# Optimization experiments

Measured on AMD Instinct MI355X. Metric: run time of the kernel, lower is better.

## Reference

```python
import jax, jax.numpy as jnp
import numpy as np

N_S, N_D, E, L = 10000, 2000, 100000, 50000
H = 8            # attention heads
H1, H2, H3 = 128, 128, 64
D_S, D_D = 128, 64
NEG_SLOPE = 0.2  # GATv2 leaky_relu slope


def setup_inputs() -> dict:
    key = jax.random.key(0)
    ks = iter(jax.random.split(key, 48))
    def nrm(shape, fan_in):
        return (jax.random.normal(next(ks), shape) / np.sqrt(fan_in)).astype(jnp.float32)
    inp = {}
    inp["x_snorna"] = jax.random.normal(next(ks), (N_S, D_S), dtype=jnp.float32)
    inp["x_disease"] = jax.random.normal(next(ks), (N_D, D_D), dtype=jnp.float32)
    inp["edge_src"] = jax.random.randint(next(ks), (E,), 0, N_S, dtype=jnp.int32)
    inp["edge_dst"] = jax.random.randint(next(ks), (E,), 0, N_D, dtype=jnp.int32)
    inp["edge_label_src"] = jax.random.randint(next(ks), (L,), 0, N_S, dtype=jnp.int32)
    inp["edge_label_dst"] = jax.random.randint(next(ks), (L,), 0, N_D, dtype=jnp.int32)
    # layer 1: GraphConv per relation (lin_rel has bias, lin_root no bias)
    inp["W1_rel_sd"] = nrm((D_S, H1), D_S); inp["b1_sd"] = jnp.zeros((H1,), jnp.float32)
    inp["W1_root_sd"] = nrm((D_D, H1), D_D)
    inp["W1_rel_ds"] = nrm((D_D, H1), D_D); inp["b1_ds"] = jnp.zeros((H1,), jnp.float32)
    inp["W1_root_ds"] = nrm((D_S, H1), D_S)
    # layer 2: GATv2Conv per relation (lin_l/lin_r with bias, att, final bias)
    for rel in ("sd", "ds"):
        inp[f"Wl2_{rel}"] = nrm((H1, H * H2), H1); inp[f"bl2_{rel}"] = jnp.zeros((H * H2,), jnp.float32)
        inp[f"Wr2_{rel}"] = nrm((H1, H * H2), H1); inp[f"br2_{rel}"] = jnp.zeros((H * H2,), jnp.float32)
        inp[f"att2_{rel}"] = nrm((H, H2), H2)
        inp[f"bias2_{rel}"] = jnp.zeros((H2,), jnp.float32)
    # layer 3: GraphConv per relation
    inp["W3_rel_sd"] = nrm((H2, H3), H2); inp["b3_sd"] = jnp.zeros((H3,), jnp.float32)
    inp["W3_root_sd"] = nrm((H2, H3), H2)
    inp["W3_rel_ds"] = nrm((H2, H3), H2); inp["b3_ds"] = jnp.zeros((H3,), jnp.float32)
    inp["W3_root_ds"] = nrm((H2, H3), H2)
    return inp


def graph_conv(x_src, x_dst, es, ed, W_rel, b_rel, W_root, n_dst):
    # PyG GraphConv: lin_rel(sum-aggregated neighbor feats) + lin_root(x_dst)
    agg = jax.ops.segment_sum(x_src[es], ed, num_segments=n_dst)
    return agg @ W_rel + b_rel + x_dst @ W_root


def gatv2(x_src, x_dst, es, ed, Wl, bl, Wr, br, att, bias, n_dst):
    # PyG GATv2Conv, bipartite, add_self_loops=False, concat=False (mean over heads)
    xl = (x_src @ Wl + bl).reshape(x_src.shape[0], H, -1)  # [Ns,H,C]
    xr = (x_dst @ Wr + br).reshape(x_dst.shape[0], H, -1)  # [Nd,H,C]
    xj = xl[es]                                            # [E,H,C] source msgs
    e = jax.nn.leaky_relu(xj + xr[ed], NEG_SLOPE)          # [E,H,C]
    score = jnp.einsum('ehc,hc->eh', e, att)               # [E,H]
    m = jax.ops.segment_max(score, ed, num_segments=n_dst)
    a = jnp.exp(score - m[ed])
    denom = jax.ops.segment_sum(a, ed, num_segments=n_dst)
    alpha = a / denom[ed]                                  # softmax over in-edges of dst
    out = jax.ops.segment_sum(alpha[:, :, None] * xj, ed, num_segments=n_dst)
    return out.mean(axis=1) + bias                         # concat=False -> head mean


def reference(x_snorna, x_disease, edge_src, edge_dst, edge_label_src, edge_label_dst,
              W1_rel_sd, b1_sd, W1_root_sd, W1_rel_ds, b1_ds, W1_root_ds,
              Wl2_sd, bl2_sd, Wr2_sd, br2_sd, att2_sd, bias2_sd,
              Wl2_ds, bl2_ds, Wr2_ds, br2_ds, att2_ds, bias2_ds,
              W3_rel_sd, b3_sd, W3_root_sd, W3_rel_ds, b3_ds, W3_root_ds):
    # HeteroConv layer 1 (GraphConv both directions); each type has one incoming relation
    xd = graph_conv(x_snorna, x_disease, edge_src, edge_dst, W1_rel_sd, b1_sd, W1_root_sd, N_D)
    xs = graph_conv(x_disease, x_snorna, edge_dst, edge_src, W1_rel_ds, b1_ds, W1_root_ds, N_S)
    xs, xd = jax.nn.relu(xs), jax.nn.relu(xd)  # dropout = identity (eval mode)
    # HeteroConv layer 2 (GATv2Conv both directions)
    xd2 = gatv2(xs, xd, edge_src, edge_dst, Wl2_sd, bl2_sd, Wr2_sd, br2_sd, att2_sd, bias2_sd, N_D)
    xs2 = gatv2(xd, xs, edge_dst, edge_src, Wl2_ds, bl2_ds, Wr2_ds, br2_ds, att2_ds, bias2_ds, N_S)
    xs2, xd2 = jax.nn.relu(xs2), jax.nn.relu(xd2)
    # HeteroConv layer 3 (GraphConv, no activation)
    xd3 = graph_conv(xs2, xd2, edge_src, edge_dst, W3_rel_sd, b3_sd, W3_root_sd, N_D)
    xs3 = graph_conv(xd2, xs2, edge_dst, edge_src, W3_rel_ds, b3_ds, W3_root_ds, N_S)
    # Classifier: per-pair dot product
    return (xs3[edge_label_src] * xd3[edge_label_dst]).sum(axis=-1)
```

## Files before the change

### kernel.cpp

```cpp
#include <hip/hip_runtime.h>
#include <math.h>

#define NEG 0.2f
static const int N_S = 10000, N_D = 2000, E_N = 100000, L_N = 50000;

using short8 = __attribute__((ext_vector_type(8))) short;
using f32x4  = __attribute__((ext_vector_type(4))) float;
typedef _Float16 h2 __attribute__((ext_vector_type(2)));

union U8h { uint4 u[2]; h2 h[8]; unsigned w[8]; };

__device__ inline unsigned short f2bf(float f) {
  unsigned u = __float_as_uint(f);
  u += 0x7fff + ((u >> 16) & 1);
  return (unsigned short)(u >> 16);
}
__device__ inline float bf2f(unsigned short u) {
  return __uint_as_float((unsigned)u << 16);
}
__device__ inline unsigned short f2h(float f) {
  _Float16 h = (_Float16)f;
  unsigned short r;
  __builtin_memcpy(&r, &h, 2);
  return r;
}

struct PkD { const float* W; unsigned short* P; int K, M; };
struct Pk12 { PkD d[12]; };
struct PrepArgs {
  const int *es, *ed;
  int *deg_s, *deg_d;
  const float *xs, *xd;
  unsigned short *xsb, *xdb;
  const float *att_sd, *att_ds;
  unsigned short *att16;
};
__global__ void k_prep(PrepArgs a, Pk12 g) {
  int bid = blockIdx.x, t = threadIdx.x;
  if (bid < 391) {
    int e = bid * 256 + t;
    if (e < E_N) {
      atomicAdd(&a.deg_d[a.ed[e]], 1);
      atomicAdd(&a.deg_s[a.es[e]], 1);
    }
  } else if (bid < 391 + 1375) {
    int i = (bid - 391) * 256 + t;
    const int ns4 = N_S * 32;
    if (i < ns4) {
      float4 v = ((const float4*)a.xs)[i];
      ushort4 o = {f2bf(v.x), f2bf(v.y), f2bf(v.z), f2bf(v.w)};
      ((ushort4*)a.xsb)[i] = o;
    } else {
      int j = i - ns4;
      float4 v = ((const float4*)a.xd)[j];
      ushort4 o = {f2bf(v.x), f2bf(v.y), f2bf(v.z), f2bf(v.w)};
      ((ushort4*)a.xdb)[j] = o;
    }
  } else if (bid < 391 + 1375 + 768) {
    int sub = bid - 391 - 1375;
    PkD d = g.d[sub >> 6];
    int total = d.K * d.M, mt = d.M >> 4;
    for (int tid = (sub & 63) * 256 + t; tid < total; tid += 64 * 256) {
      int r = tid & 7, l = (tid >> 3) & 63, rest = tid >> 9;
      int ct = rest % mt, kt = rest / mt;
      d.P[tid] = f2bf(d.W[(kt * 32 + (l >> 4) * 8 + r) * d.M + ct * 16 + (l & 15)]);
    }
  } else {
    int i = (bid - 391 - 1375 - 768) * 256 + t;
    float v = (i < 1024) ? a.att_sd[i] : a.att_ds[i - 1024];
    a.att16[i] = f2h(v);
  }
}

__global__ __launch_bounds__(1024) void k_scan2(int* c0, int* r0, int n0,
                                                int* c1, int* r1, int n1) {
  int* cur = blockIdx.x ? c1 : c0;
  int* rp  = blockIdx.x ? r1 : r0;
  int N    = blockIdx.x ? n1 : n0;
  __shared__ int wsum[16];
  __shared__ int carry;
  if (threadIdx.x == 0) carry = 0;
  __syncthreads();
  int lane = threadIdx.x & 63, wid = threadIdx.x >> 6;
  for (int base = 0; base < N; base += 1024) {
    int i = base + threadIdx.x;
    int v = (i < N) ? cur[i] : 0;
    int x = v;
    #pragma unroll
    for (int dd = 1; dd < 64; dd <<= 1) {
      int t = __shfl_up(x, dd);
      if (lane >= dd) x += t;
    }
    if (lane == 63) wsum[wid] = x;
    __syncthreads();
    int woff = 0;
    for (int ww = 0; ww < wid; ++ww) woff += wsum[ww];
    int excl = carry + woff + x - v;
    if (i < N) { rp[i] = excl; cur[i] = excl; }
    __syncthreads();
    if (threadIdx.x == 0) {
      int t = 0;
      #pragma unroll
      for (int ww = 0; ww < 16; ++ww) t += wsum[ww];
      if (base + 1024 >= N) rp[N] = carry + t;
      carry += t;
    }
    __syncthreads();
  }
}

__global__ void k_scat2(const int* __restrict__ es, const int* __restrict__ ed,
                        int* __restrict__ cur_d, int* __restrict__ cur_s,
                        int* __restrict__ csrc_d, int* __restrict__ csrc_s, int E) {
  int e = blockIdx.x * 256 + threadIdx.x;
  if (e >= E) return;
  int s = es[e], d = ed[e];
  csrc_d[atomicAdd(&cur_d[d], 1)] = s;
  csrc_s[atomicAdd(&cur_s[s], 1)] = d;
}

__device__ __forceinline__ void gath128(const unsigned short* __restrict__ x,
                                        const int* __restrict__ rp, const int* __restrict__ cs,
                                        unsigned short* __restrict__ out,
                                        int n, int half, int cl) {
  int b = rp[n], e = rp[n + 1];
  float a0 = 0.f, a1 = 0.f, a2 = 0.f, a3 = 0.f;
  int i = b + half;
  for (; i + 2 < e; i += 4) {
    uint2 v0 = *(const uint2*)(x + (long long)cs[i] * 128 + cl * 4);
    uint2 v1 = *(const uint2*)(x + (long long)cs[i + 2] * 128 + cl * 4);
    a0 += bf2f((unsigned short)(v0.x & 0xffff)) + bf2f((unsigned short)(v1.x & 0xffff));
    a1 += bf2f((unsigned short)(v0.x >> 16))    + bf2f((unsigned short)(v1.x >> 16));
    a2 += bf2f((unsigned short)(v0.y & 0xffff)) + bf2f((unsigned short)(v1.y & 0xffff));
    a3 += bf2f((unsigned short)(v0.y >> 16))    + bf2f((unsigned short)(v1.y >> 16));
  }
  for (; i < e; i += 2) {
    uint2 v0 = *(const uint2*)(x + (long long)cs[i] * 128 + cl * 4);
    a0 += bf2f((unsigned short)(v0.x & 0xffff));
    a1 += bf2f((unsigned short)(v0.x >> 16));
    a2 += bf2f((unsigned short)(v0.y & 0xffff));
    a3 += bf2f((unsigned short)(v0.y >> 16));
  }
  a0 += __shfl_xor(a0, 32); a1 += __shfl_xor(a1, 32);
  a2 += __shfl_xor(a2, 32); a3 += __shfl_xor(a3, 32);
  if (!half) {
    ushort4 o = {f2bf(a0), f2bf(a1), f2bf(a2), f2bf(a3)};
    *(ushort4*)&out[(long long)n * 128 + cl * 4] = o;
  }
}

__global__ __launch_bounds__(256) void k_gather1(
    const unsigned short* __restrict__ xsb, const unsigned short* __restrict__ xdb,
    const int* __restrict__ rpd, const int* __restrict__ csd,
    const int* __restrict__ rps, const int* __restrict__ css,
    unsigned short* __restrict__ aggd, unsigned short* __restrict__ aggs) {
  int wv = threadIdx.x >> 6, l = threadIdx.x & 63, half = l >> 5, cl = l & 31;
  int bid = blockIdx.x;
  if (bid < 500) {
    gath128(xsb, rpd, csd, aggd, bid * 4 + wv, half, cl);
  } else {
    int n = (bid - 500) * 4 + wv;
    if (n >= N_S) return;
    int b = rps[n], e = rps[n + 1];
    float a0 = 0.f, a1 = 0.f;
    int i = b + half;
    for (; i + 2 < e; i += 4) {
      unsigned v0 = *(const unsigned*)(xdb + (long long)css[i] * 64 + cl * 2);
      unsigned v1 = *(const unsigned*)(xdb + (long long)css[i + 2] * 64 + cl * 2);
      a0 += bf2f((unsigned short)(v0 & 0xffff)) + bf2f((unsigned short)(v1 & 0xffff));
      a1 += bf2f((unsigned short)(v0 >> 16))    + bf2f((unsigned short)(v1 >> 16));
    }
    for (; i < e; i += 2) {
      unsigned v0 = *(const unsigned*)(xdb + (long long)css[i] * 64 + cl * 2);
      a0 += bf2f((unsigned short)(v0 & 0xffff));
      a1 += bf2f((unsigned short)(v0 >> 16));
    }
    a0 += __shfl_xor(a0, 32); a1 += __shfl_xor(a1, 32);
    if (!half) {
      ushort2 o = {f2bf(a0), f2bf(a1)};
      *(ushort2*)&aggs[(long long)n * 64 + cl * 2] = o;
    }
  }
}

__global__ __launch_bounds__(256) void k_gather3(
    const unsigned short* __restrict__ xs2b, const unsigned short* __restrict__ xd2b,
    const int* __restrict__ rpd, const int* __restrict__ csd,
    const int* __restrict__ rps, const int* __restrict__ css,
    unsigned short* __restrict__ aggd, unsigned short* __restrict__ aggs) {
  int wv = threadIdx.x >> 6, l = threadIdx.x & 63, half = l >> 5, cl = l & 31;
  int bid = blockIdx.x;
  if (bid < 500) {
    gath128(xs2b, rpd, csd, aggd, bid * 4 + wv, half, cl);
  } else {
    int n = (bid - 500) * 4 + wv;
    if (n >= N_S) return;
    gath128(xd2b, rps, css, aggs, n, half, cl);
  }
}

struct GD {
  const unsigned short *A0, *P0, *A1, *P1;
  const float* bias;
  void* out;
  int K0, K1, N, M, relu, outmode, y0;
};
template<int ND> struct GDs { GD d[ND]; };

template<int ND>
__global__ __launch_bounds__(256) void k_mfma(GDs<ND> g) {
  int by = blockIdx.y;
  int di = 0;
  #pragma unroll
  for (int i = 1; i < ND; ++i) if (by >= g.d[i].y0) di = i;
  GD d = g.d[di];
  int ytile = by - d.y0;
  int c0 = blockIdx.x * 64;
  if (c0 >= d.M) return;
  int w = threadIdx.x >> 6, l = threadIdx.x & 63;
  int r0 = ytile * 64 + w * 16;
  if (r0 >= d.N) return;
  int lg = l >> 4, lo = l & 15;
  f32x4 acc[4] = {};
  int arow = r0 + lo; arow = (arow < d.N) ? arow : (d.N - 1);
  int mt = d.M >> 4;
  int ct0 = c0 >> 4;
  const unsigned short* a0 = d.A0 + (long long)arow * d.K0 + lg * 8;
  for (int kt = 0; kt < (d.K0 >> 5); ++kt) {
    short8 a = *(const short8*)(a0 + kt * 32);
    #pragma unroll
    for (int ct = 0; ct < 4; ++ct) {
      short8 b = *(const short8*)(d.P0 + ((long long)(kt * mt + ct0 + ct) * 64 + l) * 8);
      acc[ct] = __builtin_amdgcn_mfma_f32_16x16x32_bf16(a, b, acc[ct], 0, 0, 0);
    }
  }
  if (d.K1) {
    const unsigned short* a1 = d.A1 + (long long)arow * d.K1 + lg * 8;
    for (int kt = 0; kt < (d.K1 >> 5); ++kt) {
      short8 a = *(const short8*)(a1 + kt * 32);
      #pragma unroll
      for (int ct = 0; ct < 4; ++ct) {
        short8 b = *(const short8*)(d.P1 + ((long long)(kt * mt + ct0 + ct) * 64 + l) * 8);
        acc[ct] = __builtin_amdgcn_mfma_f32_16x16x32_bf16(a, b, acc[ct], 0, 0, 0);
      }
    }
  }
  #pragma unroll
  for (int ct = 0; ct < 4; ++ct) {
    int col = c0 + ct * 16 + lo;
    float bv = d.bias[col];
    #pragma unroll
    for (int r = 0; r < 4; ++r) {
      int grow = r0 + lg * 4 + r;
      if (grow < d.N) {
        float v = acc[ct][r] + bv;
        if (d.relu) v = fmaxf(v, 0.f);
        if (d.outmode == 1)
          ((unsigned short*)d.out)[(long long)grow * d.M + col] = f2bf(v);
        else if (d.outmode == 2)
          ((unsigned short*)d.out)[(long long)grow * d.M + col] = f2h(v);
        else
          ((float*)d.out)[(long long)grow * d.M + col] = v;
      }
    }
  }
}

template<int WPN>
__device__ __forceinline__ void gat_node(
    const unsigned short* __restrict__ xl, const unsigned short* __restrict__ xr,
    const int* __restrict__ rowptr, const int* __restrict__ srcid,
    const unsigned short* __restrict__ att16, const float* __restrict__ bias,
    unsigned short* __restrict__ outb, int node, int wsub, int l,
    float (*lm)[8], float (*lss)[8], unsigned (*lacc)[8][64]) {
  int h = l >> 3, sub = l & 7;
  int cbase = h * 128 + sub * 16;
  U8h xr8, at8;
  { const uint4* p = (const uint4*)(xr + (long long)node * 1024 + cbase);
    xr8.u[0] = p[0]; xr8.u[1] = p[1]; }
  { const uint4* p = (const uint4*)(att16 + cbase);
    at8.u[0] = p[0]; at8.u[1] = p[1]; }
  const h2 neg2 = {(_Float16)NEG, (_Float16)NEG};
  float m = -INFINITY, s = 0.f;
  h2 acc2[8] = {};
  int b = rowptr[node], e = rowptr[node + 1];

  auto process = [&](U8h& x) {
    float sc = 0.f;
    #pragma unroll
    for (int j = 0; j < 8; ++j) {
      h2 t = x.h[j] + xr8.h[j];
      h2 lk = __builtin_elementwise_max(t, t * neg2);
      sc = __builtin_amdgcn_fdot2(lk, at8.h[j], sc, false);
    }
    sc += __shfl_xor(sc, 1); sc += __shfl_xor(sc, 2); sc += __shfl_xor(sc, 4);
    if (sc > m + 4.f) {
      float scl = __expf(m - sc);
      _Float16 sh = (_Float16)scl;
      h2 s2 = {sh, sh};
      #pragma unroll
      for (int j = 0; j < 8; ++j) acc2[j] *= s2;
      s *= scl; m = sc;
    }
    float a = __expf(sc - m);
    s += a;
    _Float16 ah = (_Float16)(a * 0.00390625f);
    h2 a2 = {ah, ah};
    #pragma unroll
    for (int j = 0; j < 8; ++j) acc2[j] = __builtin_elementwise_fma(a2, x.h[j], acc2[j]);
  };

  int i = b + wsub;
  U8h c, d;
  bool hc = (i < e), hd = (i + WPN < e);
  if (hc) { const uint4* p = (const uint4*)(xl + (long long)srcid[i] * 1024 + cbase); c.u[0] = p[0]; c.u[1] = p[1]; }
  if (hd) { const uint4* p = (const uint4*)(xl + (long long)srcid[i + WPN] * 1024 + cbase); d.u[0] = p[0]; d.u[1] = p[1]; }
  while (hc) {
    int inx = i + 2 * WPN;
    U8h n0, n1;
    bool h0 = (inx < e), h1 = (inx + WPN < e);
    if (h0) { const uint4* p = (const uint4*)(xl + (long long)srcid[inx] * 1024 + cbase); n0.u[0] = p[0]; n0.u[1] = p[1]; }
    if (h1) { const uint4* p = (const uint4*)(xl + (long long)srcid[inx + WPN] * 1024 + cbase); n1.u[0] = p[0]; n1.u[1] = p[1]; }
    process(c);
    if (hd) process(d);
    c = n0; d = n1; hc = h0; hd = h1; i = inx;
  }

  float val[16];
  if constexpr (WPN == 4) {
    if (sub == 0) { lm[wsub][h] = m; lss[wsub][h] = s; }
    U8h tmp;
    #pragma unroll
    for (int j = 0; j < 8; ++j) tmp.h[j] = acc2[j];
    #pragma unroll
    for (int j = 0; j < 8; ++j) lacc[wsub][j][l] = tmp.w[j];
    __syncthreads();
    if (wsub != 0) return;
    float M2 = fmaxf(fmaxf(lm[0][h], lm[1][h]), fmaxf(lm[2][h], lm[3][h]));
    float S = 0.f;
    #pragma unroll
    for (int j = 0; j < 16; ++j) val[j] = 0.f;
    #pragma unroll
    for (int w2 = 0; w2 < 4; ++w2) {
      float scw = (M2 == -INFINITY) ? 0.f : __expf(lm[w2][h] - M2);
      S = fmaf(scw, lss[w2][h], S);
      #pragma unroll
      for (int j = 0; j < 8; ++j) {
        unsigned uw = lacc[w2][j][l];
        h2 hv; __builtin_memcpy(&hv, &uw, 4);
        val[2 * j]     = fmaf(scw, (float)hv[0], val[2 * j]);
        val[2 * j + 1] = fmaf(scw, (float)hv[1], val[2 * j + 1]);
      }
    }
    float inv = (S > 0.f) ? 256.f / S : 0.f;
    #pragma unroll
    for (int j = 0; j < 16; ++j) val[j] *= inv;
  } else {
    float inv = (s > 0.f) ? 256.f / s : 0.f;
    #pragma unroll
    for (int j = 0; j < 8; ++j) {
      val[2 * j]     = (float)acc2[j][0] * inv;
      val[2 * j + 1] = (float)acc2[j][1] * inv;
    }
  }
  #pragma unroll
  for (int j = 0; j < 16; ++j) {
    val[j] += __shfl_xor(val[j], 8);
    val[j] += __shfl_xor(val[j], 16);
    val[j] += __shfl_xor(val[j], 32);
  }
  if (l < 8) {
    #pragma unroll
    for (int q = 0; q < 4; ++q) {
      float4 bq = *(const float4*)&bias[sub * 16 + q * 4];
      ushort4 o;
      o.x = f2bf(fmaxf(val[q * 4 + 0] * 0.125f + bq.x, 0.f));
      o.y = f2bf(fmaxf(val[q * 4 + 1] * 0.125f + bq.y, 0.f));
      o.z = f2bf(fmaxf(val[q * 4 + 2] * 0.125f + bq.z, 0.f));
      o.w = f2bf(fmaxf(val[q * 4 + 3] * 0.125f + bq.w, 0.f));
      *(ushort4*)&outb[(long long)node * 128 + sub * 16 + q * 4] = o;
    }
  }
}

__global__ __launch_bounds__(256) void k_gat_both(
    const unsigned short* __restrict__ XLsd, const unsigned short* __restrict__ XRsd,
    const int* __restrict__ rpd, const int* __restrict__ csd,
    const unsigned short* __restrict__ att_sd, const float* __restrict__ bias_sd,
    unsigned short* __restrict__ XD2b,
    const unsigned short* __restrict__ XLds, const unsigned short* __restrict__ XRds,
    const int* __restrict__ rps, const int* __restrict__ css,
    const unsigned short* __restrict__ att_ds, const float* __restrict__ bias_ds,
    unsigned short* __restrict__ XS2b) {
  __shared__ float lm[4][8], lss[4][8];
  __shared__ unsigned lacc[4][8][64];
  int widx = threadIdx.x >> 6, l = threadIdx.x & 63;
  if (blockIdx.x < (unsigned)N_D) {
    gat_node<4>(XLsd, XRsd, rpd, csd, att_sd, bias_sd, XD2b,
                blockIdx.x, widx, l, lm, lss, lacc);
  } else {
    int node = (blockIdx.x - N_D) * 4 + widx;
    if (node < N_S)
      gat_node<1>(XLds, XRds, rps, css, att_ds, bias_ds, XS2b,
                  node, 0, l, lm, lss, lacc);
  }
}

__global__ void k_dot64(const float* __restrict__ xs, const float* __restrict__ xd,
                        const int* __restrict__ ls, const int* __restrict__ ld,
                        float* __restrict__ out, int L) {
  long long t = (long long)blockIdx.x * blockDim.x + threadIdx.x;
  int wave = (int)(t >> 6), lane = (int)(t & 63);
  int q = lane >> 4, sub = lane & 15;
  int eidx = wave * 4 + q;
  if (eidx >= L) return;
  const float4* a = (const float4*)(xs + (long long)ls[eidx] * 64);
  const float4* b = (const float4*)(xd + (long long)ld[eidx] * 64);
  float4 va = a[sub], vb = b[sub];
  float v = va.x * vb.x + va.y * vb.y + va.z * vb.z + va.w * vb.w;
  v += __shfl_xor(v, 1); v += __shfl_xor(v, 2);
  v += __shfl_xor(v, 4); v += __shfl_xor(v, 8);
  if (sub == 0) out[eidx] = v;
}

extern "C" void kernel_launch(void* const* d_in, const int* in_sizes, int n_in,
                              void* d_out, int out_size, void* d_ws, size_t ws_size,
                              hipStream_t stream) {
  const float* x_s = (const float*)d_in[0];
  const float* x_d = (const float*)d_in[1];
  const int* esrc = (const int*)d_in[2];
  const int* edst = (const int*)d_in[3];
  const int* lsrc = (const int*)d_in[4];
  const int* ldst = (const int*)d_in[5];
  const float* W1rel_sd  = (const float*)d_in[6];
  const float* b1_sd     = (const float*)d_in[7];
  const float* W1root_sd = (const float*)d_in[8];
  const float* W1rel_ds  = (const float*)d_in[9];
  const float* b1_ds     = (const float*)d_in[10];
  const float* W1root_ds = (const float*)d_in[11];
  const float *Wl2_sd = (const float*)d_in[12], *bl2_sd = (const float*)d_in[13],
              *Wr2_sd = (const float*)d_in[14], *br2_sd = (const float*)d_in[15],
              *att2_sd = (const float*)d_in[16], *bias2_sd = (const float*)d_in[17];
  const float *Wl2_ds = (const float*)d_in[18], *bl2_ds = (const float*)d_in[19],
              *Wr2_ds = (const float*)d_in[20], *br2_ds = (const float*)d_in[21],
              *att2_ds = (const float*)d_in[22], *bias2_ds = (const float*)d_in[23];
  const float *W3rel_sd = (const float*)d_in[24], *b3_sd = (const float*)d_in[25],
              *W3root_sd = (const float*)d_in[26];
  const float *W3rel_ds = (const float*)d_in[27], *b3_ds = (const float*)d_in[28],
              *W3root_ds = (const float*)d_in[29];
  float* out = (float*)d_out;

  float* w = (float*)d_ws;
  long long off = 0;
  auto alloc = [&](long long n) { float* p = w + off; off += (n + 63) & ~63LL; return p; };
  unsigned short* xsb   = (unsigned short*)alloc((long long)N_S * 64);
  unsigned short* xdb   = (unsigned short*)alloc((long long)N_D * 32);
  unsigned short* AGGDb = (unsigned short*)alloc((long long)N_D * 64);
  unsigned short* AGGSb = (unsigned short*)alloc((long long)N_S * 32);
  unsigned short* XS1b  = (unsigned short*)alloc((long long)N_S * 64);
  unsigned short* XD1b  = (unsigned short*)alloc((long long)N_D * 64);
  unsigned short* XLsd  = (unsigned short*)alloc((long long)N_S * 512);
  unsigned short* XRsd  = (unsigned short*)alloc((long long)N_D * 512);
  unsigned short* XLds  = (unsigned short*)alloc((long long)N_D * 512);
  unsigned short* XRds  = (unsigned short*)alloc((long long)N_S * 512);
  unsigned short* XS2b  = (unsigned short*)alloc((long long)N_S * 64);
  unsigned short* XD2b  = (unsigned short*)alloc((long long)N_D * 64);
  unsigned short* AGD3b = (unsigned short*)alloc((long long)N_D * 64);
  unsigned short* AGS3b = (unsigned short*)alloc((long long)N_S * 64);
  float* XS3 = alloc((long long)N_S * 64);
  float* XD3 = alloc((long long)N_D * 64);
  unsigned short* att16 = (unsigned short*)alloc(1024 + 64);
  unsigned short* pk[12];
  const int pksz[12] = {128 * 128, 64 * 128, 64 * 128, 128 * 128,
                        131072, 131072, 131072, 131072,
                        128 * 64, 128 * 64, 128 * 64, 128 * 64};
  for (int i = 0; i < 12; ++i) pk[i] = (unsigned short*)alloc(pksz[i] / 2 + 64);
  int* rowptr_d = (int*)alloc(N_D + 64);
  int* rowptr_s = (int*)alloc(N_S + 64);
  int* cur_all  = (int*)alloc(N_D + N_S + 128);
  int* cur_d = cur_all;
  int* cur_s = cur_all + N_D + 64;
  int* csrc_d = (int*)alloc(E_N);
  int* csrc_s = (int*)alloc(E_N);
  (void)ws_size; (void)in_sizes; (void)n_in; (void)out_size;

  hipMemsetAsync(cur_all, 0, (size_t)(N_D + N_S + 128) * 4, stream);
  PrepArgs pa = {esrc, edst, cur_s, cur_d, x_s, x_d, xsb, xdb, att2_sd, att2_ds, att16};
  Pk12 pkk = {{{W1rel_sd, pk[0], 128, 128}, {W1root_sd, pk[1], 64, 128},
               {W1rel_ds, pk[2], 64, 128},  {W1root_ds, pk[3], 128, 128},
               {Wl2_sd, pk[4], 128, 1024},  {Wr2_sd, pk[5], 128, 1024},
               {Wl2_ds, pk[6], 128, 1024},  {Wr2_ds, pk[7], 128, 1024},
               {W3rel_sd, pk[8], 128, 64},  {W3root_sd, pk[9], 128, 64},
               {W3rel_ds, pk[10], 128, 64}, {W3root_ds, pk[11], 128, 64}}};
  k_prep<<<2542, 256, 0, stream>>>(pa, pkk);
  k_scan2<<<2, 1024, 0, stream>>>(cur_d, rowptr_d, N_D, cur_s, rowptr_s, N_S);
  k_scat2<<<391, 256, 0, stream>>>(esrc, edst, cur_d, cur_s, csrc_d, csrc_s, E_N);

  k_gather1<<<3000, 256, 0, stream>>>(xsb, xdb, rowptr_d, csrc_d, rowptr_s, csrc_s,
                                      AGGDb, AGGSb);
  {
    GDs<2> g = {{{AGGDb, pk[0], xdb, pk[1], b1_sd, XD1b, 128, 64, N_D, 128, 1, 1, 0},
                 {AGGSb, pk[2], xsb, pk[3], b1_ds, XS1b, 64, 128, N_S, 128, 1, 1, 32}}};
    k_mfma<2><<<dim3(2, 189), 256, 0, stream>>>(g);
  }

  {
    GDs<4> g = {{{XS1b, pk[4], nullptr, nullptr, bl2_sd, XLsd, 128, 0, N_S, 1024, 0, 2, 0},
                 {XD1b, pk[5], nullptr, nullptr, br2_sd, XRsd, 128, 0, N_D, 1024, 0, 2, 157},
                 {XD1b, pk[6], nullptr, nullptr, bl2_ds, XLds, 128, 0, N_D, 1024, 0, 2, 189},
                 {XS1b, pk[7], nullptr, nullptr, br2_ds, XRds, 128, 0, N_S, 1024, 0, 2, 221}}};
    k_mfma<4><<<dim3(16, 378), 256, 0, stream>>>(g);
  }
  k_gat_both<<<N_D + (N_S + 3) / 4, 256, 0, stream>>>(
      XLsd, XRsd, rowptr_d, csrc_d, att16, bias2_sd, XD2b,
      XLds, XRds, rowptr_s, csrc_s, att16 + 1024, bias2_ds, XS2b);

  k_gather3<<<3000, 256, 0, stream>>>(XS2b, XD2b, rowptr_d, csrc_d, rowptr_s, csrc_s,
                                      AGD3b, AGS3b);
  {
    GDs<2> g = {{{AGD3b, pk[8], XD2b, pk[9], b3_sd, XD3, 128, 128, N_D, 64, 0, 0, 0},
                 {AGS3b, pk[10], XS2b, pk[11], b3_ds, XS3, 128, 128, N_S, 64, 0, 0, 32}}};
    k_mfma<2><<<dim3(1, 189), 256, 0, stream>>>(g);
  }

  k_dot64<<<(L_N * 16 + 255) / 256, 256, 0, stream>>>(XS3, XD3, lsrc, ldst, out, L_N);
}
```

Baseline: 199.8 us.

## Interleave dst/src block assignment and use branch-free clamped GAT edge loop

Block indices in the gather and GAT kernels are interleaved so heavy per-disease blocks and lighter per-snoRNA blocks mix across the grid rather than all heavy blocks launching first, aiming for better load balance and tail behaviour. The GAT edge loop now runs a computed trip count with clamped row indices, loading unconditionally and masking invalid contributions instead of guarding loads. This trades extra wasted loads and math on padding slots for fewer divergent branches and more regular memory issue. Grid sizes are changed to match the new mapping.

```diff
diff --git a/kernel.cpp b/kernel.cpp
--- a/kernel.cpp
+++ b/kernel.cpp
@@ -155,11 +155,11 @@
     const int* __restrict__ rps, const int* __restrict__ css,
     unsigned short* __restrict__ aggd, unsigned short* __restrict__ aggs) {
   int wv = threadIdx.x >> 6, l = threadIdx.x & 63, half = l >> 5, cl = l & 31;
-  int bid = blockIdx.x;
-  if (bid < 500) {
-    gath128(xsb, rpd, csd, aggd, bid * 4 + wv, half, cl);
+  int r = blockIdx.x % 6, q = blockIdx.x / 6;
+  if (r == 0) {
+    gath128(xsb, rpd, csd, aggd, q * 4 + wv, half, cl);
   } else {
-    int n = (bid - 500) * 4 + wv;
+    int n = (q * 5 + (r - 1)) * 4 + wv;
     if (n >= N_S) return;
     int b = rps[n], e = rps[n + 1];
     float a0 = 0.f, a1 = 0.f;
@@ -189,11 +189,11 @@
     const int* __restrict__ rps, const int* __restrict__ css,
     unsigned short* __restrict__ aggd, unsigned short* __restrict__ aggs) {
   int wv = threadIdx.x >> 6, l = threadIdx.x & 63, half = l >> 5, cl = l & 31;
-  int bid = blockIdx.x;
-  if (bid < 500) {
-    gath128(xs2b, rpd, csd, aggd, bid * 4 + wv, half, cl);
+  int r = blockIdx.x % 6, q = blockIdx.x / 6;
+  if (r == 0) {
+    gath128(xs2b, rpd, csd, aggd, q * 4 + wv, half, cl);
   } else {
-    int n = (bid - 500) * 4 + wv;
+    int n = (q * 5 + (r - 1)) * 4 + wv;
     if (n >= N_S) return;
     gath128(xd2b, rps, css, aggs, n, half, cl);
   }
@@ -284,8 +284,16 @@
   float m = -INFINITY, s = 0.f;
   h2 acc2[8] = {};
   int b = rowptr[node], e = rowptr[node + 1];
-
-  auto process = [&](U8h& x) {
+  int deg = e - b;
+
+  auto ldrow = [&](int idx, U8h& dst) {
+    int ic = idx < e - 1 ? idx : e - 1;
+    ic = ic > 0 ? ic : 0;
+    const uint4* p = (const uint4*)(xl + (long long)srcid[ic] * 1024 + cbase);
+    dst.u[0] = p[0]; dst.u[1] = p[1];
+  };
+
+  auto process = [&](U8h& x, bool valid) {
     float sc = 0.f;
     #pragma unroll
     for (int j = 0; j < 8; ++j) {
@@ -294,7 +302,7 @@
       sc = __builtin_amdgcn_fdot2(lk, at8.h[j], sc, false);
     }
     sc += __shfl_xor(sc, 1); sc += __shfl_xor(sc, 2); sc += __shfl_xor(sc, 4);
-    if (sc > m + 4.f) {
+    if (valid && sc > m + 4.f) {
       float scl = __expf(m - sc);
       _Float16 sh = (_Float16)scl;
       h2 s2 = {sh, sh};
@@ -303,6 +311,7 @@
       s *= scl; m = sc;
     }
     float a = __expf(sc - m);
+    a = valid ? a : 0.f;
     s += a;
     _Float16 ah = (_Float16)(a * 0.00390625f);
     h2 a2 = {ah, ah};
@@ -311,19 +320,20 @@
   };
 
   int i = b + wsub;
+  int nmine = (deg - wsub + WPN - 1) / WPN;
+  if (nmine < 0) nmine = 0;
+  int npairs = (nmine + 1) >> 1;
   U8h c, d;
-  bool hc = (i < e), hd = (i + WPN < e);
-  if (hc) { const uint4* p = (const uint4*)(xl + (long long)srcid[i] * 1024 + cbase); c.u[0] = p[0]; c.u[1] = p[1]; }
-  if (hd) { const uint4* p = (const uint4*)(xl + (long long)srcid[i + WPN] * 1024 + cbase); d.u[0] = p[0]; d.u[1] = p[1]; }
-  while (hc) {
-    int inx = i + 2 * WPN;
+  ldrow(i, c);
+  ldrow(i + WPN, d);
+  for (int it = 0; it < npairs; ++it) {
+    int j = i + 2 * WPN;
     U8h n0, n1;
-    bool h0 = (inx < e), h1 = (inx + WPN < e);
-    if (h0) { const uint4* p = (const uint4*)(xl + (long long)srcid[inx] * 1024 + cbase); n0.u[0] = p[0]; n0.u[1] = p[1]; }
-    if (h1) { const uint4* p = (const uint4*)(xl + (long long)srcid[inx + WPN] * 1024 + cbase); n1.u[0] = p[0]; n1.u[1] = p[1]; }
-    process(c);
-    if (hd) process(d);
-    c = n0; d = n1; hc = h0; hd = h1; i = inx;
+    ldrow(j, n0);
+    ldrow(j + WPN, n1);
+    process(c, i < e);
+    process(d, i + WPN < e);
+    c = n0; d = n1; i = j;
   }
 
   float val[16];
@@ -395,11 +405,12 @@
   __shared__ float lm[4][8], lss[4][8];
   __shared__ unsigned lacc[4][8][64];
   int widx = threadIdx.x >> 6, l = threadIdx.x & 63;
-  if (blockIdx.x < (unsigned)N_D) {
+  int r = blockIdx.x % 9, q = blockIdx.x / 9;
+  if (r < 4) {
     gat_node<4>(XLsd, XRsd, rpd, csd, att_sd, bias_sd, XD2b,
-                blockIdx.x, widx, l, lm, lss, lacc);
+                q * 4 + r, widx, l, lm, lss, lacc);
   } else {
-    int node = (blockIdx.x - N_D) * 4 + widx;
+    int node = (q * 5 + (r - 4)) * 4 + widx;
     if (node < N_S)
       gat_node<1>(XLds, XRds, rps, css, att_ds, bias_ds, XS2b,
                   node, 0, l, lm, lss, lacc);
@@ -511,7 +522,7 @@
                  {XS1b, pk[7], nullptr, nullptr, br2_ds, XRds, 128, 0, N_S, 1024, 0, 2, 221}}};
     k_mfma<4><<<dim3(16, 378), 256, 0, stream>>>(g);
   }
-  k_gat_both<<<N_D + (N_S + 3) / 4, 256, 0, stream>>>(
+  k_gat_both<<<4500, 256, 0, stream>>>(
       XLsd, XRsd, rowptr_d, csrc_d, att16, bias2_sd, XD2b,
       XLds, XRds, rowptr_s, csrc_s, att16 + 1024, bias2_ds, XS2b);
 
```

Measured after the change: 198.9 us. About the same (-0.4%).
